# Performance work log

Measured on AMD Instinct MI355X. Metric: run time of the kernel, lower is better.

The kernel has to match this reference:

```python
import jax, jax.numpy as jnp
import numpy as np

B, H, S, DK = 2, 16, 2048, 64

def setup_inputs() -> dict:
    key = jax.random.key(0)
    kq, kk, kv = jax.random.split(key, 3)
    shape = (B, H, S, DK)
    return {
        "multi_head_q": jax.random.normal(kq, shape, dtype=jnp.float32),
        "multi_head_k": jax.random.normal(kk, shape, dtype=jnp.float32),
        "multi_head_v": jax.random.normal(kv, shape, dtype=jnp.float32),
    }

def reference(multi_head_q, multi_head_k, multi_head_v):
    d_k = multi_head_q.shape[-1]
    scale = 1.0 / jnp.sqrt(jnp.asarray(d_k, dtype=multi_head_q.dtype))
    # scores: [B, H, S, S]
    scores = jnp.einsum("bhqd,bhkd->bhqk", multi_head_q, multi_head_k) * scale
    attn = jax.nn.softmax(scores, axis=-1)
    # z: [B, H, S, DK]
    z = jnp.einsum("bhqk,bhkd->bhqd", attn, multi_head_v)
    # transpose heads to [B, S, H, DK] then merge -> [B, S, H*DK]
    b, h, s, d = z.shape
    return jnp.swapaxes(z, 1, 2).reshape(b, s, h * d)
```

## Files before the change

### kernel.cpp

```cpp
#include <hip/hip_runtime.h>
#include <cmath>


#define S_LEN   2048
#define D_HEAD  64
#define NHEADS  16
#define NBH     32
#define TQ      128
#define TK      32
#define NTILE   (S_LEN / TK)
#define NSTREAM 2
#define HTILE   (NTILE / NSTREAM)
#define LDSTR   72
#define TILE_SH (TK * D_HEAD)
#define PAIR_SH 4096

typedef short bfrag8 __attribute__((ext_vector_type(8)));
typedef float f32x4  __attribute__((ext_vector_type(4)));
typedef float f32x16 __attribute__((ext_vector_type(16)));
typedef int   i32x2  __attribute__((ext_vector_type(2)));
typedef int   i32x4  __attribute__((ext_vector_type(4)));

static __device__ __forceinline__ int pk2bf(float a, float b) {
  unsigned short lo = __builtin_bit_cast(unsigned short, (__bf16)a);
  unsigned short hi = __builtin_bit_cast(unsigned short, (__bf16)b);
  return (int)lo | ((int)hi << 16);
}

static __device__ __forceinline__ float fexp2(float x) {
#if __has_builtin(__builtin_amdgcn_exp2f)
  return __builtin_amdgcn_exp2f(x);
#else
  return exp2f(x);
#endif
}

static __device__ __forceinline__ void gload_lds16(const short* g, short* l) {
  __builtin_amdgcn_global_load_lds(
      (const __attribute__((address_space(1))) void*)g,
      (__attribute__((address_space(3))) void*)l, 16, 0, 0);
}

__global__ __launch_bounds__(256)
void fa_prep(const float* __restrict__ K, const float* __restrict__ V,
             short* __restrict__ Kt, short* __restrict__ Vt) {
  __shared__ float fl[64][65];

  const int tid = threadIdx.x;
  int id = blockIdx.x;
  const bool isV = id >= NBH * (NTILE / 2);
  if (isV) id -= NBH * (NTILE / 2);
  const int xcd = id & 7;
  const int s   = id >> 3;
  const int bh  = xcd * 4 + (s >> 5);
  const int t   = s & 31;

  const size_t ibase = ((size_t)bh * S_LEN + t * 64) * D_HEAD;

  if (!isV) {
    short* kt = Kt + (size_t)(bh * (NTILE / 2) + t) * PAIR_SH;
#pragma unroll
    for (int p = 0; p < 2; ++p) {
      int idx = p * 256 + tid;
      int key = idx >> 3, c = idx & 7;
      const float* src = K + ibase + key * 64 + c * 8;
      float4 a = *(const float4*)src;
      float4 b = *(const float4*)(src + 4);
      i32x4 w;
      w[0] = pk2bf(a.x, a.y); w[1] = pk2bf(a.z, a.w);
      w[2] = pk2bf(b.x, b.y); w[3] = pk2bf(b.z, b.w);
      *(i32x4*)(kt + key * 64 + ((c ^ (key & 7)) * 8)) = w;
    }
  } else {
    short* vt = Vt + (size_t)(bh * (NTILE / 2) + t) * PAIR_SH;
#pragma unroll
    for (int i = 0; i < 4; ++i) {
      int e = (i * 256 + tid) * 4;
      int row = e >> 6, col = e & 63;
      float4 v = *(const float4*)(V + ibase + (size_t)row * 64 + col);
      fl[col + 0][row] = v.x;
      fl[col + 1][row] = v.y;
      fl[col + 2][row] = v.z;
      fl[col + 3][row] = v.w;
    }
    __syncthreads();
#pragma unroll
    for (int p = 0; p < 2; ++p) {
      int idx = p * 256 + tid;
      int d = idx >> 3, ck = idx & 7;
      const float* row = &fl[d][ck * 8];
      i32x4 w;
      w[0] = pk2bf(row[0], row[1]); w[1] = pk2bf(row[2], row[3]);
      w[2] = pk2bf(row[4], row[5]); w[3] = pk2bf(row[6], row[7]);
      short* dst = vt + (ck >> 2) * TILE_SH + d * 32
                      + (((ck & 3) ^ ((d >> 1) & 3)) * 8);
      *(i32x4*)dst = w;
    }
  }
}

__global__ __launch_bounds__(512, 4)
void fa_fwd3(const float* __restrict__ Q, const short* __restrict__ Kt,
             const short* __restrict__ Vt, float* __restrict__ Out) {
  __shared__ short SM[2 * NSTREAM * 4 * TILE_SH];

  const int tid    = threadIdx.x;
  const int wid    = tid >> 6;
  const int stream = wid >> 2;
  const int qw     = wid & 3;
  const int lane   = tid & 63;
  const int h      = lane >> 5;
  const int c      = lane & 31;
  const int c7     = c & 7;
  const int c13    = (c >> 1) & 3;
  const int qb     = 32 * qw;

  short* ksReg = SM + stream * 4 * TILE_SH;
  short* vsReg = SM + NSTREAM * 4 * TILE_SH + stream * 4 * TILE_SH;

  const int id   = blockIdx.x;
  const int xcd  = id & 7;
  const int slot = id >> 3;
  const int bh   = xcd * 4 + (slot >> 4);
  const int q0   = (slot & 15) * 128;

  const int t0   = stream * HTILE;

  const float qscale = 0.125f * 1.44269504088896340736f;

  const float* Qg = Q + ((size_t)bh * S_LEN + (q0 + qb + c)) * D_HEAD;
  bfrag8 qf[4];
#pragma unroll
  for (int sl = 0; sl < 4; ++sl) {
    const float* qp = Qg + 16 * sl + 8 * h;
    float4 a = *(const float4*)qp;
    float4 b = *(const float4*)(qp + 4);
    i32x4 w;
    w[0] = pk2bf(a.x * qscale, a.y * qscale);
    w[1] = pk2bf(a.z * qscale, a.w * qscale);
    w[2] = pk2bf(b.x * qscale, b.y * qscale);
    w[3] = pk2bf(b.z * qscale, b.w * qscale);
    qf[sl] = __builtin_bit_cast(bfrag8, w);
  }

  int koff[4], voff[4];
#pragma unroll
  for (int sl = 0; sl < 4; ++sl)
    koff[sl] = c * 64 + (((2 * sl + h) ^ c7) * 8);
#pragma unroll
  for (int sl2 = 0; sl2 < 2; ++sl2)
#pragma unroll
    for (int mtd = 0; mtd < 2; ++mtd)
      voff[sl2 * 2 + mtd] = (32 * mtd + c) * 32 + (((2 * sl2 + h) ^ c13) * 8);

  const short* ktb = Kt + (size_t)bh * NTILE * TILE_SH;
  const short* vtb = Vt + (size_t)bh * NTILE * TILE_SH;

  auto stage = [&](int b, int gt) {
    const int ch = qw * 512;
    gload_lds16(ktb + (size_t)gt * TILE_SH + ch + lane * 8,
                ksReg + b * TILE_SH + ch);
    gload_lds16(vtb + (size_t)gt * TILE_SH + ch + lane * 8,
                vsReg + b * TILE_SH + ch);
  };

  f32x16 acc[2];
#pragma unroll
  for (int m = 0; m < 2; ++m)
#pragma unroll
    for (int i = 0; i < 16; ++i) acc[m][i] = 0.f;

  float lrun = 0.f;

  auto qk = [&](int b, f32x16& st) {
#pragma unroll
    for (int i = 0; i < 16; ++i) st[i] = 0.f;
    const short* kb = ksReg + b * TILE_SH;
    __builtin_amdgcn_s_setprio(1);
#pragma unroll
    for (int sl = 0; sl < 4; ++sl) {
      bfrag8 af = *(const bfrag8*)&kb[koff[sl]];
      st = __builtin_amdgcn_mfma_f32_32x32x16_bf16(af, qf[sl], st, 0, 0, 0);
    }
    __builtin_amdgcn_s_setprio(0);
  };

  auto finish = [&](int b, f32x16& st) {
    float ls = 0.f;
#pragma unroll
    for (int i = 0; i < 16; ++i) {
      st[i] = fexp2(st[i]);
      ls += st[i];
    }
    lrun += ls;

    bfrag8 pf[2];
#pragma unroll
    for (int hf = 0; hf < 2; ++hf) {
      const int b0 = 8 * hf;
      int w0 = pk2bf(st[b0 + 0], st[b0 + 1]);
      int w1 = pk2bf(st[b0 + 2], st[b0 + 3]);
      int w2 = pk2bf(st[b0 + 4], st[b0 + 5]);
      int w3 = pk2bf(st[b0 + 6], st[b0 + 7]);
      asm("v_permlane32_swap_b32 %0, %1" : "+v"(w0), "+v"(w2));
      asm("v_permlane32_swap_b32 %0, %1" : "+v"(w1), "+v"(w3));
      i32x4 f; f[0] = w0; f[1] = w1; f[2] = w2; f[3] = w3;
      pf[hf] = __builtin_bit_cast(bfrag8, f);
    }

    const short* vb = vsReg + b * TILE_SH;
    __builtin_amdgcn_s_setprio(1);
#pragma unroll
    for (int sl2 = 0; sl2 < 2; ++sl2)
#pragma unroll
      for (int mtd = 0; mtd < 2; ++mtd) {
        bfrag8 av = *(const bfrag8*)&vb[voff[sl2 * 2 + mtd]];
        acc[mtd] = __builtin_amdgcn_mfma_f32_32x32x16_bf16(av, pf[sl2], acc[mtd], 0, 0, 0);
      }
    __builtin_amdgcn_s_setprio(0);
  };

  stage(0, t0 + 0);
  stage(1, t0 + 1);
  f32x16 stA, stB;
#pragma unroll 4
  for (int t = 0; t < HTILE; ++t) {
    if (t + 1 < HTILE) asm volatile("s_waitcnt vmcnt(2)" ::: "memory");
    else               asm volatile("s_waitcnt vmcnt(0)" ::: "memory");
    __builtin_amdgcn_s_barrier();
    __builtin_amdgcn_sched_barrier(0);
    if (t + 2 < HTILE) stage((t + 2) & 3, t0 + t + 2);
    if (t & 1) {
      qk(t & 3, stB);
      if (t > 0) finish((t - 1) & 3, stA);
    } else {
      qk(t & 3, stA);
      if (t > 0) finish((t - 1) & 3, stB);
    }
  }
  finish((HTILE - 1) & 3, stB);

  float* red = (float*)SM;
  const int rbase = (qw * 64 + lane) * 33;
  __syncthreads();
  if (stream == 1) {
#pragma unroll
    for (int i = 0; i < 16; ++i) red[rbase + i]      = acc[0][i];
#pragma unroll
    for (int i = 0; i < 16; ++i) red[rbase + 16 + i] = acc[1][i];
    red[rbase + 32] = lrun;
  }
  __syncthreads();
  if (stream == 0) {
#pragma unroll
    for (int i = 0; i < 16; ++i) acc[0][i] += red[rbase + i];
#pragma unroll
    for (int i = 0; i < 16; ++i) acc[1][i] += red[rbase + 16 + i];
    lrun += red[rbase + 32];
    float l = lrun + __shfl_xor(lrun, 32);
    float inv = 1.0f / l;
    const int bb = bh >> 4, hh = bh & 15;
    const int qg = q0 + qb + c;
    float* op = Out + ((size_t)bb * S_LEN + qg) * (NHEADS * D_HEAD) + hh * D_HEAD;
#pragma unroll
    for (int mtd = 0; mtd < 2; ++mtd)
#pragma unroll
      for (int g = 0; g < 4; ++g) {
        float4 o;
        o.x = acc[mtd][4 * g + 0] * inv;
        o.y = acc[mtd][4 * g + 1] * inv;
        o.z = acc[mtd][4 * g + 2] * inv;
        o.w = acc[mtd][4 * g + 3] * inv;
        *(float4*)(op + 32 * mtd + 8 * g + 4 * h) = o;
      }
  }
}

__global__ __launch_bounds__(256, 2)
void fa_fwd(const float* __restrict__ Q, const float* __restrict__ K,
            const float* __restrict__ V, float* __restrict__ Out) {
  __shared__ short Ksf[2][64 * LDSTR];
  __shared__ short VsT[2][D_HEAD * LDSTR];
  __shared__ short Psf[TQ * LDSTR];

  const int tid  = threadIdx.x;
  const int wid  = tid >> 6;
  const int lane = tid & 63;
  const int quad = lane >> 4;
  const int r    = lane & 15;
  const int qb   = 32 * wid;

  const int bh = blockIdx.y;
  const int q0 = blockIdx.x * TQ;

  const float* Qg = Q + (size_t)bh * S_LEN * D_HEAD;
  const float* Kg = K + (size_t)bh * S_LEN * D_HEAD;
  const float* Vg = V + (size_t)bh * S_LEN * D_HEAD;

  const float qscale = 0.125f * 1.44269504088896340736f;

  bfrag8 qf[2][2];
#pragma unroll
  for (int nt = 0; nt < 2; ++nt)
#pragma unroll
    for (int ks = 0; ks < 2; ++ks) {
      const float* qp = Qg + (size_t)(q0 + qb + 16 * nt + r) * D_HEAD + 32 * ks + 8 * quad;
      float4 a = *(const float4*)qp;
      float4 b = *(const float4*)(qp + 4);
      i32x4 w;
      w[0] = pk2bf(a.x * qscale, a.y * qscale);
      w[1] = pk2bf(a.z * qscale, a.w * qscale);
      w[2] = pk2bf(b.x * qscale, b.y * qscale);
      w[3] = pk2bf(b.z * qscale, b.w * qscale);
      qf[nt][ks] = __builtin_bit_cast(bfrag8, w);
    }

  float4 kpre[4];
  float  vpre[16];

  auto load_tile = [&](int k0) {
#pragma unroll
    for (int i = 0; i < 4; ++i) {
      int e = (i * 256 + tid) * 4;
      kpre[i] = *(const float4*)(Kg + (size_t)(k0 + (e >> 6)) * D_HEAD + (e & 63));
    }
    const float* vpp = Vg + (size_t)(k0 + wid * 16) * D_HEAD + lane;
#pragma unroll
    for (int j = 0; j < 16; ++j) vpre[j] = vpp[(size_t)j * D_HEAD];
  };

  auto store_tile = [&](short* ksb, short* vsb) {
#pragma unroll
    for (int i = 0; i < 4; ++i) {
      int e = (i * 256 + tid) * 4;
      i32x2 w;
      w[0] = pk2bf(kpre[i].x, kpre[i].y);
      w[1] = pk2bf(kpre[i].z, kpre[i].w);
      *(i32x2*)&ksb[(e >> 6) * LDSTR + (e & 63)] = w;
    }
    i32x4 w0, w1;
#pragma unroll
    for (int j = 0; j < 4; ++j) w0[j] = pk2bf(vpre[2 * j],     vpre[2 * j + 1]);
#pragma unroll
    for (int j = 0; j < 4; ++j) w1[j] = pk2bf(vpre[8 + 2 * j], vpre[9 + 2 * j]);
    *(i32x4*)&vsb[lane * LDSTR + wid * 16]     = w0;
    *(i32x4*)&vsb[lane * LDSTR + wid * 16 + 8] = w1;
  };

  f32x4 acc[4][2];
#pragma unroll
  for (int mt = 0; mt < 4; ++mt)
#pragma unroll
    for (int nt = 0; nt < 2; ++nt)
      acc[mt][nt] = (f32x4){0.f, 0.f, 0.f, 0.f};

  float lrun[2] = {0.f, 0.f};

  auto compute = [&](const short* ksb, const short* vsb) {
    f32x4 st[4][2];
#pragma unroll
    for (int mt = 0; mt < 4; ++mt)
#pragma unroll
      for (int nt = 0; nt < 2; ++nt)
        st[mt][nt] = (f32x4){0.f, 0.f, 0.f, 0.f};
#pragma unroll
    for (int ks = 0; ks < 2; ++ks) {
      bfrag8 af[4];
#pragma unroll
      for (int mt = 0; mt < 4; ++mt)
        af[mt] = *(const bfrag8*)&ksb[(r + 16 * mt) * LDSTR + quad * 8 + 32 * ks];
#pragma unroll
      for (int mt = 0; mt < 4; ++mt)
#pragma unroll
        for (int nt = 0; nt < 2; ++nt)
          st[mt][nt] = __builtin_amdgcn_mfma_f32_16x16x32_bf16(af[mt], qf[nt][ks], st[mt][nt], 0, 0, 0);
    }
#pragma unroll
    for (int nt = 0; nt < 2; ++nt) {
      float ssum = 0.f;
#pragma unroll
      for (int mt = 0; mt < 4; ++mt) {
        float p0 = fexp2(st[mt][nt][0]);
        float p1 = fexp2(st[mt][nt][1]);
        float p2 = fexp2(st[mt][nt][2]);
        float p3 = fexp2(st[mt][nt][3]);
        ssum += (p0 + p1) + (p2 + p3);
        i32x2 w;
        w[0] = pk2bf(p0, p1);
        w[1] = pk2bf(p2, p3);
        *(i32x2*)&Psf[(qb + 16 * nt + r) * LDSTR + 16 * mt + 4 * quad] = w;
      }
      lrun[nt] += ssum;
    }
#pragma unroll
    for (int ks = 0; ks < 2; ++ks) {
      bfrag8 av[4], bp[2];
#pragma unroll
      for (int mt = 0; mt < 4; ++mt)
        av[mt] = *(const bfrag8*)&vsb[(r + 16 * mt) * LDSTR + quad * 8 + 32 * ks];
#pragma unroll
      for (int nt = 0; nt < 2; ++nt)
        bp[nt] = *(const bfrag8*)&Psf[(qb + 16 * nt + r) * LDSTR + quad * 8 + 32 * ks];
#pragma unroll
      for (int mt = 0; mt < 4; ++mt)
#pragma unroll
        for (int nt = 0; nt < 2; ++nt)
          acc[mt][nt] = __builtin_amdgcn_mfma_f32_16x16x32_bf16(av[mt], bp[nt], acc[mt][nt], 0, 0, 0);
    }
  };

  load_tile(0);
  store_tile(Ksf[0], VsT[0]);
  load_tile(64);

  for (int it = 0; it < S_LEN / 64; it += 2) {
    __syncthreads();
    compute(Ksf[0], VsT[0]);
    store_tile(Ksf[1], VsT[1]);
    if (it + 2 < S_LEN / 64) load_tile((it + 2) * 64);
    __syncthreads();
    compute(Ksf[1], VsT[1]);
    if (it + 2 < S_LEN / 64) {
      store_tile(Ksf[0], VsT[0]);
      if (it + 3 < S_LEN / 64) load_tile((it + 3) * 64);
    }
  }

  const int bb = bh >> 4, hh = bh & 15;
#pragma unroll
  for (int nt = 0; nt < 2; ++nt) {
    float l = lrun[nt];
    l += __shfl_xor(l, 16);
    l += __shfl_xor(l, 32);
    float inv = 1.0f / l;
    int qg = q0 + qb + 16 * nt + r;
    float* op = Out + ((size_t)bb * S_LEN + qg) * (NHEADS * D_HEAD) + hh * D_HEAD;
#pragma unroll
    for (int mt = 0; mt < 4; ++mt) {
      float4 o;
      o.x = acc[mt][nt][0] * inv; o.y = acc[mt][nt][1] * inv;
      o.z = acc[mt][nt][2] * inv; o.w = acc[mt][nt][3] * inv;
      *(float4*)(op + 16 * mt + 4 * quad) = o;
    }
  }
}

extern "C" void kernel_launch(void* const* d_in, const int* in_sizes, int n_in,
                              void* d_out, int out_size, void* d_ws, size_t ws_size,
                              hipStream_t stream) {
  const float* Q = (const float*)d_in[0];
  const float* K = (const float*)d_in[1];
  const float* V = (const float*)d_in[2];
  float* O = (float*)d_out;

  const size_t telems = (size_t)NBH * NTILE * TILE_SH;
  const size_t need   = 2 * telems * sizeof(short);

  if (ws_size >= need) {
    short* Kt = (short*)d_ws;
    short* Vt = Kt + telems;
    fa_prep<<<dim3(NBH * NTILE), 256, 0, stream>>>(K, V, Kt, Vt);
    fa_fwd3<<<dim3(512), 512, 0, stream>>>(Q, Kt, Vt, O);
  } else {
    dim3 grid(S_LEN / TQ, NBH);
    fa_fwd<<<grid, 256, 0, stream>>>(Q, K, V, O);
  }
}
```

Before: 134.4 us.

## Process two KV tiles per barrier with a five-slot rotating LDS ring

Reworks the attention main loop so each barrier covers two K/V tiles instead of one. A five-buffer LDS ring with rotating offsets replaces the four-buffer modulo indexing, which halves the number of barriers and waitcnt points per stream. Exp2 becomes an inline v_exp_f32 with an s_nop, and the row-sum is computed as a tree to shorten the dependency chain. In exchange the kernel uses more LDS, which may reduce occupancy, and the waits are now a full vmcnt(0) drain each iteration rather than a partial wait.

After: 237.8 us. 76.9% more time.

```diff
diff --git a/kernel.cpp b/kernel.cpp
--- a/kernel.cpp
+++ b/kernel.cpp
@@ -28,11 +28,9 @@
 }
 
 static __device__ __forceinline__ float fexp2(float x) {
-#if __has_builtin(__builtin_amdgcn_exp2f)
-  return __builtin_amdgcn_exp2f(x);
-#else
-  return exp2f(x);
-#endif
+  float r;
+  asm("v_exp_f32 %0, %1\n\ts_nop 0" : "=v"(r) : "v"(x));
+  return r;
 }
 
 static __device__ __forceinline__ void gload_lds16(const short* g, short* l) {
@@ -102,7 +100,7 @@
 __global__ __launch_bounds__(512, 4)
 void fa_fwd3(const float* __restrict__ Q, const short* __restrict__ Kt,
              const short* __restrict__ Vt, float* __restrict__ Out) {
-  __shared__ short SM[2 * NSTREAM * 4 * TILE_SH];
+  __shared__ short SM[2 * NSTREAM * 5 * TILE_SH];
 
   const int tid    = threadIdx.x;
   const int wid    = tid >> 6;
@@ -115,8 +113,8 @@
   const int c13    = (c >> 1) & 3;
   const int qb     = 32 * qw;
 
-  short* ksReg = SM + stream * 4 * TILE_SH;
-  short* vsReg = SM + NSTREAM * 4 * TILE_SH + stream * 4 * TILE_SH;
+  short* ksBase = SM + stream * 5 * TILE_SH;
+  short* vsBase = SM + NSTREAM * 5 * TILE_SH + stream * 5 * TILE_SH;
 
   const int id   = blockIdx.x;
   const int xcd  = id & 7;
@@ -156,12 +154,11 @@
   const short* ktb = Kt + (size_t)bh * NTILE * TILE_SH;
   const short* vtb = Vt + (size_t)bh * NTILE * TILE_SH;
 
-  auto stage = [&](int b, int gt) {
+  auto stage = [&](int boff, int t) {
+    const int gt = t0 + t;
     const int ch = qw * 512;
-    gload_lds16(ktb + (size_t)gt * TILE_SH + ch + lane * 8,
-                ksReg + b * TILE_SH + ch);
-    gload_lds16(vtb + (size_t)gt * TILE_SH + ch + lane * 8,
-                vsReg + b * TILE_SH + ch);
+    gload_lds16(ktb + (size_t)gt * TILE_SH + ch + lane * 8, ksBase + boff + ch);
+    gload_lds16(vtb + (size_t)gt * TILE_SH + ch + lane * 8, vsBase + boff + ch);
   };
 
   f32x16 acc[2];
@@ -172,10 +169,10 @@
 
   float lrun = 0.f;
 
-  auto qk = [&](int b, f32x16& st) {
+  auto qk = [&](int boff, f32x16& st) {
 #pragma unroll
     for (int i = 0; i < 16; ++i) st[i] = 0.f;
-    const short* kb = ksReg + b * TILE_SH;
+    const short* kb = ksBase + boff;
     __builtin_amdgcn_s_setprio(1);
 #pragma unroll
     for (int sl = 0; sl < 4; ++sl) {
@@ -185,30 +182,31 @@
     __builtin_amdgcn_s_setprio(0);
   };
 
-  auto finish = [&](int b, f32x16& st) {
-    float ls = 0.f;
-#pragma unroll
-    for (int i = 0; i < 16; ++i) {
-      st[i] = fexp2(st[i]);
-      ls += st[i];
-    }
-    lrun += ls;
+  auto finish = [&](int boff, f32x16& st) {
+    float p[16];
+#pragma unroll
+    for (int i = 0; i < 16; ++i) p[i] = fexp2(st[i]);
+    float s0 = (p[0] + p[1]) + (p[2] + p[3]);
+    float s1 = (p[4] + p[5]) + (p[6] + p[7]);
+    float s2 = (p[8] + p[9]) + (p[10] + p[11]);
+    float s3 = (p[12] + p[13]) + (p[14] + p[15]);
+    lrun += (s0 + s1) + (s2 + s3);
 
     bfrag8 pf[2];
 #pragma unroll
     for (int hf = 0; hf < 2; ++hf) {
       const int b0 = 8 * hf;
-      int w0 = pk2bf(st[b0 + 0], st[b0 + 1]);
-      int w1 = pk2bf(st[b0 + 2], st[b0 + 3]);
-      int w2 = pk2bf(st[b0 + 4], st[b0 + 5]);
-      int w3 = pk2bf(st[b0 + 6], st[b0 + 7]);
+      int w0 = pk2bf(p[b0 + 0], p[b0 + 1]);
+      int w1 = pk2bf(p[b0 + 2], p[b0 + 3]);
+      int w2 = pk2bf(p[b0 + 4], p[b0 + 5]);
+      int w3 = pk2bf(p[b0 + 6], p[b0 + 7]);
       asm("v_permlane32_swap_b32 %0, %1" : "+v"(w0), "+v"(w2));
       asm("v_permlane32_swap_b32 %0, %1" : "+v"(w1), "+v"(w3));
       i32x4 f; f[0] = w0; f[1] = w1; f[2] = w2; f[3] = w3;
       pf[hf] = __builtin_bit_cast(bfrag8, f);
     }
 
-    const short* vb = vsReg + b * TILE_SH;
+    const short* vb = vsBase + boff;
     __builtin_amdgcn_s_setprio(1);
 #pragma unroll
     for (int sl2 = 0; sl2 < 2; ++sl2)
@@ -220,25 +218,37 @@
     __builtin_amdgcn_s_setprio(0);
   };
 
-  stage(0, t0 + 0);
-  stage(1, t0 + 1);
+  stage(0 * TILE_SH, 0);
+  stage(1 * TILE_SH, 1);
   f32x16 stA, stB;
-#pragma unroll 4
-  for (int t = 0; t < HTILE; ++t) {
-    if (t + 1 < HTILE) asm volatile("s_waitcnt vmcnt(2)" ::: "memory");
-    else               asm volatile("s_waitcnt vmcnt(0)" ::: "memory");
+
+  asm volatile("s_waitcnt vmcnt(0)" ::: "memory");
+  __builtin_amdgcn_s_barrier();
+  __builtin_amdgcn_sched_barrier(0);
+  stage(2 * TILE_SH, 2);
+  stage(3 * TILE_SH, 3);
+  qk(0 * TILE_SH, stA);
+  qk(1 * TILE_SH, stB);
+  finish(0 * TILE_SH, stA);
+
+  int rb0 = 1 * TILE_SH, rb1 = 2 * TILE_SH, rb2 = 3 * TILE_SH,
+      rb3 = 4 * TILE_SH, rb4 = 0 * TILE_SH;
+
+#pragma unroll 5
+  for (int w = 2; w < HTILE; w += 2) {
+    asm volatile("s_waitcnt vmcnt(0)" ::: "memory");
     __builtin_amdgcn_s_barrier();
     __builtin_amdgcn_sched_barrier(0);
-    if (t + 2 < HTILE) stage((t + 2) & 3, t0 + t + 2);
-    if (t & 1) {
-      qk(t & 3, stB);
-      if (t > 0) finish((t - 1) & 3, stA);
-    } else {
-      qk(t & 3, stA);
-      if (t > 0) finish((t - 1) & 3, stB);
-    }
-  }
-  finish((HTILE - 1) & 3, stB);
+    if (w + 2 < HTILE) stage(rb3, w + 2);
+    if (w + 3 < HTILE) stage(rb4, w + 3);
+    qk(rb1, stA);
+    finish(rb0, stB);
+    qk(rb2, stB);
+    finish(rb1, stA);
+    int x0 = rb0, x1 = rb1;
+    rb0 = rb2; rb1 = rb3; rb2 = rb4; rb3 = x0; rb4 = x1;
+  }
+  finish(rb0, stB);
 
   float* red = (float*)SM;
   const int rbase = (qw * 64 + lane) * 33;
```

## Process K/V tiles in pairs per barrier with two-tile prefetch

Applied to the files above, without the earlier changes.

The main loop now handles two K/V tiles per iteration. It waits for all outstanding loads, issues prefetches for the next two tiles, then runs both QK MFMAs before both softmax/PV stages. This replaces the per-tile software pipeline, which overlapped the QK of one tile with the finish of the previous one. The change halves the number of barriers and waitcnts, at the cost of a full vmcnt(0) wait that exposes more load latency. The row-sum of exponentials is also rewritten as a tree reduction to shorten its dependency chain.

New measurement: 141.1 us. 5.0% more time.

```diff
diff --git a/kernel.cpp b/kernel.cpp
--- a/kernel.cpp
+++ b/kernel.cpp
@@ -115,8 +115,8 @@
   const int c13    = (c >> 1) & 3;
   const int qb     = 32 * qw;
 
-  short* ksReg = SM + stream * 4 * TILE_SH;
-  short* vsReg = SM + NSTREAM * 4 * TILE_SH + stream * 4 * TILE_SH;
+  short* ksBase = SM + stream * 4 * TILE_SH;
+  short* vsBase = SM + NSTREAM * 4 * TILE_SH + stream * 4 * TILE_SH;
 
   const int id   = blockIdx.x;
   const int xcd  = id & 7;
@@ -156,12 +156,13 @@
   const short* ktb = Kt + (size_t)bh * NTILE * TILE_SH;
   const short* vtb = Vt + (size_t)bh * NTILE * TILE_SH;
 
-  auto stage = [&](int b, int gt) {
+  auto stage = [&](int b, int t) {
+    const int gt = t0 + t;
     const int ch = qw * 512;
     gload_lds16(ktb + (size_t)gt * TILE_SH + ch + lane * 8,
-                ksReg + b * TILE_SH + ch);
+                ksBase + b * TILE_SH + ch);
     gload_lds16(vtb + (size_t)gt * TILE_SH + ch + lane * 8,
-                vsReg + b * TILE_SH + ch);
+                vsBase + b * TILE_SH + ch);
   };
 
   f32x16 acc[2];
@@ -175,7 +176,7 @@
   auto qk = [&](int b, f32x16& st) {
 #pragma unroll
     for (int i = 0; i < 16; ++i) st[i] = 0.f;
-    const short* kb = ksReg + b * TILE_SH;
+    const short* kb = ksBase + b * TILE_SH;
     __builtin_amdgcn_s_setprio(1);
 #pragma unroll
     for (int sl = 0; sl < 4; ++sl) {
@@ -186,13 +187,13 @@
   };
 
   auto finish = [&](int b, f32x16& st) {
-    float ls = 0.f;
-#pragma unroll
-    for (int i = 0; i < 16; ++i) {
-      st[i] = fexp2(st[i]);
-      ls += st[i];
-    }
-    lrun += ls;
+#pragma unroll
+    for (int i = 0; i < 16; ++i) st[i] = fexp2(st[i]);
+    float s0 = (st[0] + st[1]) + (st[2] + st[3]);
+    float s1 = (st[4] + st[5]) + (st[6] + st[7]);
+    float s2 = (st[8] + st[9]) + (st[10] + st[11]);
+    float s3 = (st[12] + st[13]) + (st[14] + st[15]);
+    lrun += (s0 + s1) + (s2 + s3);
 
     bfrag8 pf[2];
 #pragma unroll
@@ -208,7 +209,7 @@
       pf[hf] = __builtin_bit_cast(bfrag8, f);
     }
 
-    const short* vb = vsReg + b * TILE_SH;
+    const short* vb = vsBase + b * TILE_SH;
     __builtin_amdgcn_s_setprio(1);
 #pragma unroll
     for (int sl2 = 0; sl2 < 2; ++sl2)
@@ -220,25 +221,21 @@
     __builtin_amdgcn_s_setprio(0);
   };
 
-  stage(0, t0 + 0);
-  stage(1, t0 + 1);
-  f32x16 stA, stB;
-#pragma unroll 4
-  for (int t = 0; t < HTILE; ++t) {
-    if (t + 1 < HTILE) asm volatile("s_waitcnt vmcnt(2)" ::: "memory");
-    else               asm volatile("s_waitcnt vmcnt(0)" ::: "memory");
+  stage(0, 0);
+  stage(1, 1);
+#pragma unroll 2
+  for (int w = 0; w < HTILE; w += 2) {
+    asm volatile("s_waitcnt vmcnt(0)" ::: "memory");
     __builtin_amdgcn_s_barrier();
     __builtin_amdgcn_sched_barrier(0);
-    if (t + 2 < HTILE) stage((t + 2) & 3, t0 + t + 2);
-    if (t & 1) {
-      qk(t & 3, stB);
-      if (t > 0) finish((t - 1) & 3, stA);
-    } else {
-      qk(t & 3, stA);
-      if (t > 0) finish((t - 1) & 3, stB);
-    }
-  }
-  finish((HTILE - 1) & 3, stB);
+    if (w + 2 < HTILE) stage((w + 2) & 3, w + 2);
+    if (w + 3 < HTILE) stage((w + 3) & 3, w + 3);
+    f32x16 stA, stB;
+    qk(w & 3, stA);
+    qk((w + 1) & 3, stB);
+    finish(w & 3, stA);
+    finish((w + 1) & 3, stB);
+  }
 
   float* red = (float*)SM;
   const int rbase = (qw * 64 + lane) * 33;
```
